# Kernel tuning notes

Hardware: AMD Instinct MI355X
Metric: run time of the kernel (lower is better)

## Reference

```python
import jax, jax.numpy as jnp
import numpy as np

N, E = 50000, 800000
IN, H, OUT = 500, 128, 64


def _gcn_layer(x, src, dst, norm, W, b):
    # Linear transform first (PyG GCNConv applies lin before propagate)
    h = x @ W                                   # [N, F_out]
    msg = norm[:, None] * h[src]                # [E', F_out] gather
    out = jax.ops.segment_sum(msg, dst, num_segments=N)  # scatter-add
    return out + b


def setup_inputs() -> dict:
    key = jax.random.key(0)
    k = jax.random.split(key, 6)
    x = jax.random.normal(k[0], (N, IN), jnp.float32)
    edge_index = jax.random.randint(k[1], (2, E), 0, N, dtype=jnp.int32)
    # Glorot-style init like PyG GCNConv
    W1 = jax.random.normal(k[2], (IN, H), jnp.float32) * (1.0 / np.sqrt(IN))
    b1 = jnp.zeros((H,), jnp.float32)
    W2 = jax.random.normal(k[3], (H, OUT), jnp.float32) * (1.0 / np.sqrt(H))
    b2 = jnp.zeros((OUT,), jnp.float32)
    return {"x": x, "edge_index": edge_index, "W1": W1, "b1": b1, "W2": W2, "b2": b2}


def reference(x, edge_index, W1, b1, W2, b2):
    # Add self loops (PyG GCNConv default add_self_loops=True)
    loops = jnp.arange(N, dtype=edge_index.dtype)
    src = jnp.concatenate([edge_index[0], loops])
    dst = jnp.concatenate([edge_index[1], loops])
    # Symmetric degree normalization: deg computed on targets (col)
    deg = jax.ops.segment_sum(jnp.ones_like(src, dtype=x.dtype), dst, num_segments=N)
    dis = jnp.where(deg > 0, jax.lax.rsqrt(jnp.maximum(deg, 1.0)), 0.0)
    norm = dis[src] * dis[dst]                  # [E+N]
    h = jax.nn.relu(_gcn_layer(x, src, dst, norm, W1, b1))
    return _gcn_layer(h, src, dst, norm, W2, b2)
```

## Files before the change

### kernel.cpp

```cpp
#include <hip/hip_runtime.h>
#include <hip/hip_bf16.h>


typedef __attribute__((ext_vector_type(4))) float f32x4;
typedef __attribute__((ext_vector_type(8))) short short8;
typedef __attribute__((ext_vector_type(8))) unsigned short u16x8;

static __device__ __forceinline__ unsigned short f2bf(float f) {
    unsigned int u = __float_as_uint(f);
    u += 0x7FFF + ((u >> 16) & 1);
    return (unsigned short)(u >> 16);
}
static __device__ __forceinline__ float bf2f(unsigned short h) {
    return __uint_as_float(((unsigned int)h) << 16);
}

__global__ void deg_accum_i(const int* __restrict__ dst, int* __restrict__ deg, int E) {
    int i = blockIdx.x * blockDim.x + threadIdx.x;
    if (i < E) atomicAdd(&deg[dst[i]], 1);
}

__global__ void prep_and_zero(const float* __restrict__ W1, const float* __restrict__ W2,
                              unsigned short* __restrict__ B1h, unsigned short* __restrict__ B1l,
                              unsigned short* __restrict__ B2h, unsigned short* __restrict__ B2l,
                              int* __restrict__ deg, int Nn,
                              int K1, int N1, int K1p, int K2, int N2, int K2p) {
    int idx = blockIdx.x * 256 + threadIdx.x;
    if (idx < Nn) deg[idx] = 0;
    int n1 = N1 * K1p;
    if (idx < n1) {
        int n = idx / K1p, k = idx - n * K1p;
        float v = (k < K1) ? W1[(size_t)k * N1 + n] : 0.f;
        unsigned short h = f2bf(v);
        B1h[idx] = h;
        B1l[idx] = f2bf(v - bf2f(h));
    } else {
        int idx2 = idx - n1;
        if (idx2 < N2 * K2p) {
            int n = idx2 / K2p, k = idx2 - n * K2p;
            float v = (k < K2) ? W2[(size_t)k * N2 + n] : 0.f;
            unsigned short h = f2bf(v);
            B2h[idx2] = h;
            B2l[idx2] = f2bf(v - bf2f(h));
        }
    }
}

__global__ void scan_part(const int* __restrict__ deg, int* __restrict__ bsum, int N) {
    int tid = threadIdx.x, lane = tid & 63, wid = tid >> 6;
    int i = blockIdx.x * 256 + tid;
    int v = (i < N) ? deg[i] : 0;
#pragma unroll
    for (int off = 1; off < 64; off <<= 1) v += __shfl_xor(v, off, 64);
    __shared__ int ws[4];
    if (lane == 0) ws[wid] = v;
    __syncthreads();
    if (tid == 0) bsum[blockIdx.x] = ws[0] + ws[1] + ws[2] + ws[3];
}

__global__ __launch_bounds__(1024) void scan_top(const int* __restrict__ bsum, int nb,
                                                 int* __restrict__ boff, int* __restrict__ rp, int N) {
    __shared__ int wsum[16];
    int tid = threadIdx.x, lane = tid & 63, wid = tid >> 6;
    int v = (tid < nb) ? bsum[tid] : 0;
    int x = v;
#pragma unroll
    for (int off = 1; off < 64; off <<= 1) {
        int t = __shfl_up(x, off, 64);
        if (lane >= off) x += t;
    }
    if (lane == 63) wsum[wid] = x;
    __syncthreads();
    if (tid < 16) {
        int y = wsum[tid];
#pragma unroll
        for (int off = 1; off < 16; off <<= 1) {
            int t = __shfl_up(y, off, 16);
            if (tid >= off) y += t;
        }
        wsum[tid] = y;
    }
    __syncthreads();
    int base = wid ? wsum[wid - 1] : 0;
    if (tid < nb) boff[tid] = base + x - v;
    if (tid == 0) rp[N] = wsum[15];
}

__global__ void scan_final(int* __restrict__ deg, const int* __restrict__ boff,
                           int* __restrict__ rp, int* __restrict__ cursor, int N) {
    int tid = threadIdx.x, lane = tid & 63, wid = tid >> 6;
    int i = blockIdx.x * 256 + tid;
    int v = (i < N) ? deg[i] : 0;
    int x = v;
#pragma unroll
    for (int off = 1; off < 64; off <<= 1) {
        int t = __shfl_up(x, off, 64);
        if (lane >= off) x += t;
    }
    __shared__ int wsum[4];
    if (lane == 63) wsum[wid] = x;
    __syncthreads();
    int base = boff[blockIdx.x];
    for (int ww = 0; ww < wid; ww++) base += wsum[ww];
    int ex = base + x - v;
    if (i < N) {
        rp[i] = ex;
        cursor[i] = ex;
        ((float*)deg)[i] = rsqrtf((float)(v + 1));
    }
}

__global__ void csr_fill(const int* __restrict__ src, const int* __restrict__ dst,
                         int* __restrict__ cursor, int* __restrict__ csr_src, int E) {
    int e = blockIdx.x * blockDim.x + threadIdx.x;
    if (e < E) {
        int pos = atomicAdd(&cursor[dst[e]], 1);
        csr_src[pos] = src[e];
    }
}

template<int BN, int KT, int WROWS, int WCOLS>
__global__ __launch_bounds__(256) void gemm_mfma(
    const float* __restrict__ A, const unsigned short* __restrict__ Bth,
    const unsigned short* __restrict__ Btl, unsigned short* __restrict__ C,
    int M, int K, int Kpad) {
    constexpr int BM = 32, BK = 32, STR = BK + 8;
    constexpr int MF = (BM / WROWS) / 16;
    constexpr int NF = (BN / WCOLS) / 16;
    constexpr int TPB = 256 / BN;
    constexpr int BCH = BK / TPB;
    constexpr int NV = BCH / 8;
    static_assert(BN * TPB == 256 && NV >= 1, "B staging mapping");

    __shared__ unsigned short AsH[BM][STR], AsL[BM][STR];
    __shared__ unsigned short BsH[BN][STR], BsL[BN][STR];

    const int tid = threadIdx.x;
    const int lane = tid & 63;
    const int w = tid >> 6;
    const int wrow = (w / WCOLS) * (BM / WROWS);
    const int wcol = (w % WCOLS) * (BN / WCOLS);
    const int bm = blockIdx.x * BM;
    const int lrow = lane & 15;
    const int lkq = (lane >> 4) * 8;
    const int ar = tid >> 3;
    const int ak = (tid & 7) << 2;
    const int bn = tid / TPB;
    const int bkoff = (tid % TPB) * BCH;

    f32x4 acc[MF][NF] = {};

    float4 areg[KT];
    {
        const int arow = bm + ar;
        const bool rok = arow < M;
        const float* rowp = &A[(size_t)arow * K];
#pragma unroll
        for (int kt = 0; kt < KT; kt++) {
            int kg = kt * 32 + ak;
            float4 v = make_float4(0.f, 0.f, 0.f, 0.f);
            if (rok) {
                if (kg + 3 < K) v = *(const float4*)&rowp[kg];
                else {
                    if (kg     < K) v.x = rowp[kg];
                    if (kg + 1 < K) v.y = rowp[kg + 1];
                    if (kg + 2 < K) v.z = rowp[kg + 2];
                }
            }
            areg[kt] = v;
        }
    }

    u16x8 bh[NV], bl[NV];
    auto loadB = [&](int kt) {
        const size_t bo = (size_t)bn * Kpad + kt * 32 + bkoff;
#pragma unroll
        for (int v = 0; v < NV; v++) {
            bh[v] = *(const u16x8*)&Bth[bo + v * 8];
            bl[v] = *(const u16x8*)&Btl[bo + v * 8];
        }
    };
    loadB(0);

    for (int kt = 0; kt < KT; kt++) {
        {
            float4 v = areg[kt];
            ushort4 h4, l4;
            h4.x = f2bf(v.x); l4.x = f2bf(v.x - bf2f(h4.x));
            h4.y = f2bf(v.y); l4.y = f2bf(v.y - bf2f(h4.y));
            h4.z = f2bf(v.z); l4.z = f2bf(v.z - bf2f(h4.z));
            h4.w = f2bf(v.w); l4.w = f2bf(v.w - bf2f(h4.w));
            *(ushort4*)&AsH[ar][ak] = h4;
            *(ushort4*)&AsL[ar][ak] = l4;
        }
#pragma unroll
        for (int v = 0; v < NV; v++) {
            *(u16x8*)&BsH[bn][bkoff + v * 8] = bh[v];
            *(u16x8*)&BsL[bn][bkoff + v * 8] = bl[v];
        }
        __syncthreads();
        if (kt + 1 < KT) loadB(kt + 1);
        short8 ah[MF], al[MF], bhf[NF], blf[NF];
#pragma unroll
        for (int m = 0; m < MF; m++) {
            ah[m] = *(const short8*)&AsH[wrow + m * 16 + lrow][lkq];
            al[m] = *(const short8*)&AsL[wrow + m * 16 + lrow][lkq];
        }
#pragma unroll
        for (int n = 0; n < NF; n++) {
            bhf[n] = *(const short8*)&BsH[wcol + n * 16 + lrow][lkq];
            blf[n] = *(const short8*)&BsL[wcol + n * 16 + lrow][lkq];
        }
#pragma unroll
        for (int m = 0; m < MF; m++)
#pragma unroll
            for (int n = 0; n < NF; n++) {
                acc[m][n] = __builtin_amdgcn_mfma_f32_16x16x32_bf16(ah[m], bhf[n], acc[m][n], 0, 0, 0);
                acc[m][n] = __builtin_amdgcn_mfma_f32_16x16x32_bf16(al[m], bhf[n], acc[m][n], 0, 0, 0);
                acc[m][n] = __builtin_amdgcn_mfma_f32_16x16x32_bf16(ah[m], blf[n], acc[m][n], 0, 0, 0);
            }
        __syncthreads();
    }
#pragma unroll
    for (int m = 0; m < MF; m++)
#pragma unroll
        for (int n = 0; n < NF; n++)
#pragma unroll
            for (int q = 0; q < 4; q++) {
                int row = bm + wrow + m * 16 + (lane >> 4) * 4 + q;
                int col = wcol + n * 16 + (lane & 15);
                if (row < M) C[(size_t)row * BN + col] = f2bf(acc[m][n][q]);
            }
}

__global__ __launch_bounds__(256) void gather128(
    const int* __restrict__ rp, const int* __restrict__ csr,
    const float* __restrict__ dis, const unsigned short* __restrict__ h,
    const float* __restrict__ bias, float* __restrict__ out, int Nn) {
    int n = (blockIdx.x * 256 + threadIdx.x) >> 6;
    int lane = threadIdx.x & 63;
    if (n >= Nn) return;
    const int hh = lane >> 5;
    const int l = lane & 31;
    int beg = rp[n], end = rp[n + 1];
    float4 a0 = {0,0,0,0}, a1 = {0,0,0,0}, a2 = {0,0,0,0}, a3 = {0,0,0,0};
    auto P = [&](int e, float4& a) {
        int s = csr[e];
        float w = dis[s];
        ushort4 v = *(const ushort4*)&h[(size_t)s * 128 + l * 4];
        a.x = fmaf(w, bf2f(v.x), a.x); a.y = fmaf(w, bf2f(v.y), a.y);
        a.z = fmaf(w, bf2f(v.z), a.z); a.w = fmaf(w, bf2f(v.w), a.w);
    };
    int j = beg + hh;
    for (; j + 6 < end; j += 8) { P(j, a0); P(j + 2, a1); P(j + 4, a2); P(j + 6, a3); }
    for (; j < end; j += 2) P(j, a0);
    float4 acc;
    acc.x = (a0.x + a1.x) + (a2.x + a3.x);
    acc.y = (a0.y + a1.y) + (a2.y + a3.y);
    acc.z = (a0.z + a1.z) + (a2.z + a3.z);
    acc.w = (a0.w + a1.w) + (a2.w + a3.w);
    acc.x += __shfl_xor(acc.x, 32);
    acc.y += __shfl_xor(acc.y, 32);
    acc.z += __shfl_xor(acc.z, 32);
    acc.w += __shfl_xor(acc.w, 32);
    float dn = dis[n];
    ushort4 hv = *(const ushort4*)&h[(size_t)n * 128 + l * 4];
    float4 b4 = *(const float4*)&bias[l * 4];
    float4 o;
    o.x = fmaxf(dn * (acc.x + dn * bf2f(hv.x)) + b4.x, 0.f);
    o.y = fmaxf(dn * (acc.y + dn * bf2f(hv.y)) + b4.y, 0.f);
    o.z = fmaxf(dn * (acc.z + dn * bf2f(hv.z)) + b4.z, 0.f);
    o.w = fmaxf(dn * (acc.w + dn * bf2f(hv.w)) + b4.w, 0.f);
    if (hh == 0) *(float4*)&out[(size_t)n * 128 + l * 4] = o;
}

__global__ __launch_bounds__(256) void gather64(
    const int* __restrict__ rp, const int* __restrict__ csr,
    const float* __restrict__ dis, const unsigned short* __restrict__ h,
    const float* __restrict__ bias, float* __restrict__ out, int Nn) {
    int n = (blockIdx.x * 256 + threadIdx.x) >> 6;
    int lane = threadIdx.x & 63;
    if (n >= Nn) return;
    const int q = lane >> 4;
    const int l = lane & 15;
    int beg = rp[n], end = rp[n + 1];
    float4 a0 = {0,0,0,0}, a1 = {0,0,0,0};
    auto P = [&](int e, float4& a) {
        int s = csr[e];
        float w = dis[s];
        ushort4 v = *(const ushort4*)&h[(size_t)s * 64 + l * 4];
        a.x = fmaf(w, bf2f(v.x), a.x); a.y = fmaf(w, bf2f(v.y), a.y);
        a.z = fmaf(w, bf2f(v.z), a.z); a.w = fmaf(w, bf2f(v.w), a.w);
    };
    int j = beg + q;
    for (; j + 4 < end; j += 8) { P(j, a0); P(j + 4, a1); }
    for (; j < end; j += 4) P(j, a0);
    float4 acc;
    acc.x = a0.x + a1.x; acc.y = a0.y + a1.y;
    acc.z = a0.z + a1.z; acc.w = a0.w + a1.w;
    acc.x += __shfl_xor(acc.x, 16); acc.x += __shfl_xor(acc.x, 32);
    acc.y += __shfl_xor(acc.y, 16); acc.y += __shfl_xor(acc.y, 32);
    acc.z += __shfl_xor(acc.z, 16); acc.z += __shfl_xor(acc.z, 32);
    acc.w += __shfl_xor(acc.w, 16); acc.w += __shfl_xor(acc.w, 32);
    float dn = dis[n];
    ushort4 hv = *(const ushort4*)&h[(size_t)n * 64 + l * 4];
    float4 b4 = *(const float4*)&bias[l * 4];
    float4 o;
    o.x = dn * (acc.x + dn * bf2f(hv.x)) + b4.x;
    o.y = dn * (acc.y + dn * bf2f(hv.y)) + b4.y;
    o.z = dn * (acc.z + dn * bf2f(hv.z)) + b4.z;
    o.w = dn * (acc.w + dn * bf2f(hv.w)) + b4.w;
    if (q == 0) *(float4*)&out[(size_t)n * 64 + l * 4] = o;
}

extern "C" void kernel_launch(void* const* d_in, const int* in_sizes, int n_in,
                              void* d_out, int out_size, void* d_ws, size_t ws_size,
                              hipStream_t stream) {
    const float* x  = (const float*)d_in[0];
    const int*   ei = (const int*)d_in[1];
    const float* W1 = (const float*)d_in[2];
    const float* b1 = (const float*)d_in[3];
    const float* W2 = (const float*)d_in[4];
    const float* b2 = (const float*)d_in[5];

    const int IN = 500, H = 128, OUT = 64;
    const int Nn = in_sizes[0] / IN;
    const int E  = in_sizes[1] / 2;
    const int* src  = ei;
    const int* dstp = ei + E;

    const int Npad = ((Nn + 63) / 64) * 64;
    const int nb   = (Nn + 255) / 256;
    const int K1p  = 512, K2p = 128;

    int*   degdis  = (int*)d_ws;
    int*   rp      = degdis + Npad;
    int*   bsum    = rp + Npad + 64;
    int*   boff    = bsum + 1024;
    int*   cursor  = boff + 1024;
    int*   csr_src = cursor + Npad;
    unsigned short* Bt1h = (unsigned short*)(csr_src + ((E + 63) / 64) * 64);
    unsigned short* Bt1l = Bt1h + H * K1p;
    unsigned short* Bt2h = Bt1l + H * K1p;
    unsigned short* Bt2l = Bt2h + OUT * K2p;
    unsigned short* h1u  = Bt2l + OUT * K2p;
    float* agg1    = (float*)(h1u + (size_t)Nn * H);
    unsigned short* h2u  = h1u;
    float* dis     = (float*)degdis;
    float* out     = (float*)d_out;

    prep_and_zero<<<(H * K1p + OUT * K2p + 255) / 256, 256, 0, stream>>>(
        W1, W2, Bt1h, Bt1l, Bt2h, Bt2l, degdis, Nn, IN, H, K1p, H, OUT, K2p);
    deg_accum_i<<<(E + 255) / 256, 256, 0, stream>>>(dstp, degdis, E);
    scan_part<<<nb, 256, 0, stream>>>(degdis, bsum, Nn);
    scan_top<<<1, 1024, 0, stream>>>(bsum, nb, boff, rp, Nn);
    scan_final<<<nb, 256, 0, stream>>>(degdis, boff, rp, cursor, Nn);
    csr_fill<<<(E + 255) / 256, 256, 0, stream>>>(src, dstp, cursor, csr_src, E);

    gemm_mfma<128, 16, 2, 2><<<(Nn + 31) / 32, 256, 0, stream>>>(x, Bt1h, Bt1l, h1u, Nn, IN, K1p);
    gather128<<<(Nn + 3) / 4, 256, 0, stream>>>(rp, csr_src, dis, h1u, b1, agg1, Nn);

    gemm_mfma<64, 4, 2, 2><<<(Nn + 31) / 32, 256, 0, stream>>>(agg1, Bt2h, Bt2l, h2u, Nn, H, K2p);
    gather64<<<(Nn + 3) / 4, 256, 0, stream>>>(rp, csr_src, dis, h2u, b2, out, Nn);
}
```

Baseline: 218.4 us.

## Rewrite split-bf16 GEMMs to use direct global-to-LDS loads with double buffering

Replaces the register-staged MFMA GEMM with a kernel that copies fp32 A tiles and pre-split bf16 weight images straight into LDS using global_load_lds, double-buffered so the next K tile loads while the current one computes. Weights are pre-arranged into a tile-major hi/lo image so each 1KB chunk maps directly to LDS. The row tile grows from 32 to 64 and the A split into hi/lo moves to the compute step. The final partial K tile of layer 1 goes through registers for masking. This adds conversion work per compute step and relies on clamping out-of-range rows.

```diff
diff --git a/kernel.cpp b/kernel.cpp
--- a/kernel.cpp
+++ b/kernel.cpp
@@ -4,7 +4,6 @@
 
 typedef __attribute__((ext_vector_type(4))) float f32x4;
 typedef __attribute__((ext_vector_type(8))) short short8;
-typedef __attribute__((ext_vector_type(8))) unsigned short u16x8;
 
 static __device__ __forceinline__ unsigned short f2bf(float f) {
     unsigned int u = __float_as_uint(f);
@@ -15,33 +14,42 @@
     return __uint_as_float(((unsigned int)h) << 16);
 }
 
+static __device__ __forceinline__ void glds16(const void* g, void* l) {
+    __builtin_amdgcn_global_load_lds(
+        (const __attribute__((address_space(1))) void*)g,
+        (__attribute__((address_space(3))) void*)l, 16, 0, 0);
+}
+
 __global__ void deg_accum_i(const int* __restrict__ dst, int* __restrict__ deg, int E) {
     int i = blockIdx.x * blockDim.x + threadIdx.x;
     if (i < E) atomicAdd(&deg[dst[i]], 1);
 }
 
-__global__ void prep_and_zero(const float* __restrict__ W1, const float* __restrict__ W2,
-                              unsigned short* __restrict__ B1h, unsigned short* __restrict__ B1l,
-                              unsigned short* __restrict__ B2h, unsigned short* __restrict__ B2l,
-                              int* __restrict__ deg, int Nn,
-                              int K1, int N1, int K1p, int K2, int N2, int K2p) {
+__global__ void prep_imgs(const float* __restrict__ W1, const float* __restrict__ W2,
+                          unsigned short* __restrict__ I1, unsigned short* __restrict__ I2,
+                          int* __restrict__ deg, int Nn) {
     int idx = blockIdx.x * 256 + threadIdx.x;
     if (idx < Nn) deg[idx] = 0;
-    int n1 = N1 * K1p;
-    if (idx < n1) {
-        int n = idx / K1p, k = idx - n * K1p;
-        float v = (k < K1) ? W1[(size_t)k * N1 + n] : 0.f;
-        unsigned short h = f2bf(v);
-        B1h[idx] = h;
-        B1l[idx] = f2bf(v - bf2f(h));
-    } else {
-        int idx2 = idx - n1;
-        if (idx2 < N2 * K2p) {
-            int n = idx2 / K2p, k = idx2 - n * K2p;
-            float v = (k < K2) ? W2[(size_t)k * N2 + n] : 0.f;
+    const int total1 = 16 * 1024;
+    if (idx < total1) {
+        int kt = idx >> 10, pl = (idx >> 9) & 1, slot = (idx >> 7) & 3, col = idx & 127;
+        int k0 = kt * 32 + slot * 8;
+#pragma unroll
+        for (int j = 0; j < 8; j++) {
+            int k = k0 + j;
+            float v = (k < 500) ? W1[(size_t)k * 128 + col] : 0.f;
             unsigned short h = f2bf(v);
-            B2h[idx2] = h;
-            B2l[idx2] = f2bf(v - bf2f(h));
+            I1[(size_t)idx * 8 + j] = pl ? f2bf(v - bf2f(h)) : h;
+        }
+    } else if (idx < total1 + 2048) {
+        int i2 = idx - total1;
+        int kt = i2 >> 9, pl = (i2 >> 8) & 1, slot = (i2 >> 6) & 3, col = i2 & 63;
+        int k0 = kt * 32 + slot * 8;
+#pragma unroll
+        for (int j = 0; j < 8; j++) {
+            float v = W2[(size_t)(k0 + j) * 64 + col];
+            unsigned short h = f2bf(v);
+            I2[(size_t)i2 * 8 + j] = pl ? f2bf(v - bf2f(h)) : h;
         }
     }
 }
@@ -119,110 +127,123 @@
     }
 }
 
-template<int BN, int KT, int WROWS, int WCOLS>
-__global__ __launch_bounds__(256) void gemm_mfma(
-    const float* __restrict__ A, const unsigned short* __restrict__ Bth,
-    const unsigned short* __restrict__ Btl, unsigned short* __restrict__ C,
-    int M, int K, int Kpad) {
-    constexpr int BM = 32, BK = 32, STR = BK + 8;
-    constexpr int MF = (BM / WROWS) / 16;
-    constexpr int NF = (BN / WCOLS) / 16;
-    constexpr int TPB = 256 / BN;
-    constexpr int BCH = BK / TPB;
-    constexpr int NV = BCH / 8;
-    static_assert(BN * TPB == 256 && NV >= 1, "B staging mapping");
-
-    __shared__ unsigned short AsH[BM][STR], AsL[BM][STR];
-    __shared__ unsigned short BsH[BN][STR], BsL[BN][STR];
-
-    const int tid = threadIdx.x;
-    const int lane = tid & 63;
-    const int w = tid >> 6;
-    const int wrow = (w / WCOLS) * (BM / WROWS);
-    const int wcol = (w % WCOLS) * (BN / WCOLS);
-    const int bm = blockIdx.x * BM;
-    const int lrow = lane & 15;
-    const int lkq = (lane >> 4) * 8;
-    const int ar = tid >> 3;
-    const int ak = (tid & 7) << 2;
-    const int bn = tid / TPB;
-    const int bkoff = (tid % TPB) * BCH;
-
-    f32x4 acc[MF][NF] = {};
-
-    float4 areg[KT];
-    {
-        const int arow = bm + ar;
-        const bool rok = arow < M;
-        const float* rowp = &A[(size_t)arow * K];
-#pragma unroll
-        for (int kt = 0; kt < KT; kt++) {
-            int kg = kt * 32 + ak;
-            float4 v = make_float4(0.f, 0.f, 0.f, 0.f);
-            if (rok) {
-                if (kg + 3 < K) v = *(const float4*)&rowp[kg];
-                else {
-                    if (kg     < K) v.x = rowp[kg];
-                    if (kg + 1 < K) v.y = rowp[kg + 1];
-                    if (kg + 2 < K) v.z = rowp[kg + 2];
-                }
-            }
-            areg[kt] = v;
-        }
-    }
-
-    u16x8 bh[NV], bl[NV];
-    auto loadB = [&](int kt) {
-        const size_t bo = (size_t)bn * Kpad + kt * 32 + bkoff;
-#pragma unroll
-        for (int v = 0; v < NV; v++) {
-            bh[v] = *(const u16x8*)&Bth[bo + v * 8];
-            bl[v] = *(const u16x8*)&Btl[bo + v * 8];
-        }
-    };
-    loadB(0);
-
+template<int BN, int KT, int KFULL>
+__global__ __launch_bounds__(256) void gemm_glds(
+    const float* __restrict__ A, const unsigned char* __restrict__ Wimg,
+    unsigned short* __restrict__ C, int M, int K) {
+    constexpr int ABYTES = 64 * 32 * 4;
+    constexpr int BBYTES = BN * 32 * 2 * 2;
+    constexpr int STEP = ABYTES + BBYTES;
+    constexpr int AINST = ABYTES / 1024;
+    constexpr int BINST = BBYTES / 1024;
+    constexpr int IPW = (AINST + BINST) / 4;
+    constexpr int BIPW = BINST / 4;
+    constexpr int NF = BN / 32;
+
+    __shared__ unsigned char smem[2][STEP];
+
+    const int tid = threadIdx.x, lane = tid & 63, w = tid >> 6;
+    const int lrow = lane & 15, lq = lane >> 4;
+    const int wrow = (w >> 1) * 32;
+    const int wcol = (w & 1) * (BN / 2);
+    const int bm = blockIdx.x * 64;
+
+    f32x4 acc[2][NF] = {};
+
+    float pr[8];
+    if constexpr (KFULL < KT) {
+        const int prow = tid >> 2, pk = (tid & 3) * 8;
+        const int grow = bm + prow;
+#pragma unroll
+        for (int j = 0; j < 8; j++) {
+            int k = KFULL * 32 + pk + j;
+            pr[j] = (grow < M && k < K) ? A[(size_t)grow * K + k] : 0.f;
+        }
+    }
+
+    auto STAGE = [&](int kt, int buf) {
+        unsigned char* base = &smem[buf][0];
+#pragma unroll
+        for (int j = 0; j < IPW; j++) {
+            int g = w * IPW + j;
+            if (g < AINST) {
+                int srow = bm + lane; if (srow >= M) srow = M - 1;
+                glds16(A + (size_t)srow * K + kt * 32 + g * 4, base + g * 1024);
+            } else {
+                int b = g - AINST;
+                glds16(Wimg + (size_t)kt * BBYTES + (size_t)b * 1024 + lane * 16,
+                       base + ABYTES + b * 1024);
+            }
+        }
+    };
+    auto STAGE_B = [&](int kt, int buf) {
+        unsigned char* base = &smem[buf][0];
+#pragma unroll
+        for (int j = 0; j < BIPW; j++) {
+            int b = w * BIPW + j;
+            glds16(Wimg + (size_t)kt * BBYTES + (size_t)b * 1024 + lane * 16,
+                   base + ABYTES + b * 1024);
+        }
+    };
+    auto REGWRITE = [&](int buf) {
+        const int prow = tid >> 2, pk = (tid & 3) * 8;
+        unsigned char* base = &smem[buf][0];
+        int s0 = pk >> 2;
+        *(float4*)(base + s0 * 1024 + prow * 16) = make_float4(pr[0], pr[1], pr[2], pr[3]);
+        *(float4*)(base + (s0 + 1) * 1024 + prow * 16) = make_float4(pr[4], pr[5], pr[6], pr[7]);
+    };
+    auto COMPUTE = [&](int buf) {
+        const unsigned char* base = &smem[buf][0];
+        short8 ah[2], al[2];
+#pragma unroll
+        for (int m = 0; m < 2; m++) {
+            int r = wrow + m * 16 + lrow;
+            float4 f0 = *(const float4*)(base + (lq * 2) * 1024 + r * 16);
+            float4 f1 = *(const float4*)(base + (lq * 2 + 1) * 1024 + r * 16);
+            float fv[8] = {f0.x, f0.y, f0.z, f0.w, f1.x, f1.y, f1.z, f1.w};
+#pragma unroll
+            for (int e = 0; e < 8; e++) {
+                unsigned short hu = f2bf(fv[e]);
+                ah[m][e] = (short)hu;
+                al[m][e] = (short)f2bf(fv[e] - bf2f(hu));
+            }
+        }
+        short8 bh[NF], bl[NF];
+#pragma unroll
+        for (int n = 0; n < NF; n++) {
+            int c = wcol + n * 16 + lrow;
+            bh[n] = *(const short8*)(base + ABYTES + lq * (BN * 16) + c * 16);
+            bl[n] = *(const short8*)(base + ABYTES + BBYTES / 2 + lq * (BN * 16) + c * 16);
+        }
+#pragma unroll
+        for (int m = 0; m < 2; m++)
+#pragma unroll
+            for (int n = 0; n < NF; n++) {
+                acc[m][n] = __builtin_amdgcn_mfma_f32_16x16x32_bf16(ah[m], bh[n], acc[m][n], 0, 0, 0);
+                acc[m][n] = __builtin_amdgcn_mfma_f32_16x16x32_bf16(al[m], bh[n], acc[m][n], 0, 0, 0);
+                acc[m][n] = __builtin_amdgcn_mfma_f32_16x16x32_bf16(ah[m], bl[n], acc[m][n], 0, 0, 0);
+            }
+    };
+
+    STAGE(0, 0);
+    __syncthreads();
+    int cur = 0;
     for (int kt = 0; kt < KT; kt++) {
-        {
-            float4 v = areg[kt];
-            ushort4 h4, l4;
-            h4.x = f2bf(v.x); l4.x = f2bf(v.x - bf2f(h4.x));
-            h4.y = f2bf(v.y); l4.y = f2bf(v.y - bf2f(h4.y));
-            h4.z = f2bf(v.z); l4.z = f2bf(v.z - bf2f(h4.z));
-            h4.w = f2bf(v.w); l4.w = f2bf(v.w - bf2f(h4.w));
-            *(ushort4*)&AsH[ar][ak] = h4;
-            *(ushort4*)&AsL[ar][ak] = l4;
-        }
-#pragma unroll
-        for (int v = 0; v < NV; v++) {
-            *(u16x8*)&BsH[bn][bkoff + v * 8] = bh[v];
-            *(u16x8*)&BsL[bn][bkoff + v * 8] = bl[v];
-        }
+        if (kt + 1 < KT) {
+            if constexpr (KFULL < KT) {
+                if (kt + 1 == KFULL) { STAGE_B(kt + 1, cur ^ 1); REGWRITE(cur ^ 1); }
+                else STAGE(kt + 1, cur ^ 1);
+            } else {
+                STAGE(kt + 1, cur ^ 1);
+            }
+        }
+        COMPUTE(cur);
         __syncthreads();
-        if (kt + 1 < KT) loadB(kt + 1);
-        short8 ah[MF], al[MF], bhf[NF], blf[NF];
-#pragma unroll
-        for (int m = 0; m < MF; m++) {
-            ah[m] = *(const short8*)&AsH[wrow + m * 16 + lrow][lkq];
-            al[m] = *(const short8*)&AsL[wrow + m * 16 + lrow][lkq];
-        }
-#pragma unroll
-        for (int n = 0; n < NF; n++) {
-            bhf[n] = *(const short8*)&BsH[wcol + n * 16 + lrow][lkq];
-            blf[n] = *(const short8*)&BsL[wcol + n * 16 + lrow][lkq];
-        }
-#pragma unroll
-        for (int m = 0; m < MF; m++)
-#pragma unroll
-            for (int n = 0; n < NF; n++) {
-                acc[m][n] = __builtin_amdgcn_mfma_f32_16x16x32_bf16(ah[m], bhf[n], acc[m][n], 0, 0, 0);
-                acc[m][n] = __builtin_amdgcn_mfma_f32_16x16x32_bf16(al[m], bhf[n], acc[m][n], 0, 0, 0);
-                acc[m][n] = __builtin_amdgcn_mfma_f32_16x16x32_bf16(ah[m], blf[n], acc[m][n], 0, 0, 0);
-            }
-        __syncthreads();
-    }
-#pragma unroll
-    for (int m = 0; m < MF; m++)
+        cur ^= 1;
+    }
+
+#pragma unroll
+    for (int m = 0; m < 2; m++)
 #pragma unroll
         for (int n = 0; n < NF; n++)
 #pragma unroll
@@ -331,7 +352,6 @@
 
     const int Npad = ((Nn + 63) / 64) * 64;
     const int nb   = (Nn + 255) / 256;
-    const int K1p  = 512, K2p = 128;
 
     int*   degdis  = (int*)d_ws;
     int*   rp      = degdis + Npad;
@@ -339,27 +359,26 @@
     int*   boff    = bsum + 1024;
     int*   cursor  = boff + 1024;
     int*   csr_src = cursor + Npad;
-    unsigned short* Bt1h = (unsigned short*)(csr_src + ((E + 63) / 64) * 64);
-    unsigned short* Bt1l = Bt1h + H * K1p;
-    unsigned short* Bt2h = Bt1l + H * K1p;
-    unsigned short* Bt2l = Bt2h + OUT * K2p;
-    unsigned short* h1u  = Bt2l + OUT * K2p;
-    float* agg1    = (float*)(h1u + (size_t)Nn * H);
-    unsigned short* h2u  = h1u;
+    unsigned short* I1 = (unsigned short*)(csr_src + ((E + 63) / 64) * 64);
+    unsigned short* I2 = I1 + 16 * 8192;
+    unsigned short* h1u = I2 + 4 * 4096;
+    float* agg1    = (float*)(h1u + (size_t)Npad * H);
+    unsigned short* h2u = h1u;
     float* dis     = (float*)degdis;
     float* out     = (float*)d_out;
 
-    prep_and_zero<<<(H * K1p + OUT * K2p + 255) / 256, 256, 0, stream>>>(
-        W1, W2, Bt1h, Bt1l, Bt2h, Bt2l, degdis, Nn, IN, H, K1p, H, OUT, K2p);
+    prep_imgs<<<(Nn + 255) / 256, 256, 0, stream>>>(W1, W2, I1, I2, degdis, Nn);
     deg_accum_i<<<(E + 255) / 256, 256, 0, stream>>>(dstp, degdis, E);
     scan_part<<<nb, 256, 0, stream>>>(degdis, bsum, Nn);
     scan_top<<<1, 1024, 0, stream>>>(bsum, nb, boff, rp, Nn);
     scan_final<<<nb, 256, 0, stream>>>(degdis, boff, rp, cursor, Nn);
     csr_fill<<<(E + 255) / 256, 256, 0, stream>>>(src, dstp, cursor, csr_src, E);
 
-    gemm_mfma<128, 16, 2, 2><<<(Nn + 31) / 32, 256, 0, stream>>>(x, Bt1h, Bt1l, h1u, Nn, IN, K1p);
+    gemm_glds<128, 16, 15><<<(Nn + 63) / 64, 256, 0, stream>>>(
+        x, (const unsigned char*)I1, h1u, Nn, IN);
     gather128<<<(Nn + 3) / 4, 256, 0, stream>>>(rp, csr_src, dis, h1u, b1, agg1, Nn);
 
-    gemm_mfma<64, 4, 2, 2><<<(Nn + 31) / 32, 256, 0, stream>>>(agg1, Bt2h, Bt2l, h2u, Nn, H, K2p);
+    gemm_glds<64, 4, 4><<<(Nn + 63) / 64, 256, 0, stream>>>(
+        agg1, (const unsigned char*)I2, h2u, Nn, H);
     gather64<<<(Nn + 3) / 4, 256, 0, stream>>>(rp, csr_src, dis, h2u, b2, out, Nn);
 }
```

After: 217.1 us. About the same (-0.6%).
